# Optimization experiments

Hardware: AMD Instinct MI355X
Metric: run time of the kernel (lower is better)

Reference implementation:

```python
import jax, jax.numpy as jnp
import numpy as np

WS = 8        # window_size -> N = 64
P = 8         # patch_size
HEADS = 3
DIM = 96
B = 2048


def _relative_positions_log(ws):
    coords = jnp.stack(jnp.meshgrid(jnp.arange(ws), jnp.arange(ws), indexing='ij'))  # [2,ws,ws]
    cf = coords.reshape(2, -1)                                   # [2, N]
    rel = cf[:, :, None] - cf[:, None, :]                        # [2, N, N]
    rel = rel.transpose(1, 2, 0).astype(jnp.float32)             # [N, N, 2]
    return jnp.sign(rel) * jnp.log1p(jnp.abs(rel))


def setup_inputs() -> dict:
    key = jax.random.key(0)
    k0, k1, k2 = jax.random.split(key, 3)
    N = WS * WS
    qkv = jax.random.normal(k0, (B, N, 3 * DIM), dtype=jnp.float32)
    w1 = jax.random.normal(k1, (2, 256), dtype=jnp.float32) * 0.02
    b1 = jnp.zeros((256,), dtype=jnp.float32)
    w2 = jax.random.normal(k2, (256, HEADS), dtype=jnp.float32) * 0.02
    b2 = jnp.zeros((HEADS,), dtype=jnp.float32)
    return {"qkv": qkv, "w1": w1, "b1": b1, "w2": w2, "b2": b2}


def reference(qkv, w1, b1, w2, b2):
    B_, N, C3 = qkv.shape
    dim = C3 // 3
    h = HEADS
    d = dim // h
    scale = d ** (-0.5)

    qkv = qkv.reshape(B_, N, 3, h, d).transpose(2, 0, 3, 1, 4)   # [3,B,h,N,d]
    q, k, v = qkv[0] * scale, qkv[1], qkv[2]

    c = N // (P * P)
    def to_patch(x):  # [B,h,N,d] -> [B,h,c,d,P,P]
        return x.reshape(B_, h, c, P, P, d).transpose(0, 1, 2, 5, 3, 4)

    q_fft = jnp.fft.rfft2(to_patch(q))
    k_fft = jnp.fft.rfft2(to_patch(k))
    out = jnp.fft.irfft2(q_fft * k_fft, s=(P, P))                # [B,h,c,d,P,P]
    out = out.transpose(0, 1, 2, 4, 5, 3).reshape(B_, h, N, d)   # back to [B,h,N,d]

    rp = _relative_positions_log(WS)                             # [N,N,2]
    bias = jax.nn.relu(rp @ w1 + b1) @ w2 + b2                   # [N,N,h]
    bias = bias.transpose(2, 0, 1)                               # [h,N,N]

    attn = jnp.einsum('bhnd,bhmd->bhnm', out, v) + bias[None]
    attn = jax.nn.softmax(attn, axis=-1)
    x = jnp.einsum('bhnm,bhmd->bhnd', attn, v)
    return x.transpose(0, 2, 1, 3).reshape(B_, N, dim)
```

## Files before the change

kernel.cpp:

```cpp
#include <hip/hip_runtime.h>

#define B_TOT 2048
#define NHEAD 3

typedef __attribute__((ext_vector_type(8))) short short8v;
typedef __attribute__((ext_vector_type(4))) float f32x4;
typedef __attribute__((ext_vector_type(2))) __fp16 f16x2;

typedef __attribute__((address_space(1))) const void* gas_ptr;
typedef __attribute__((address_space(3))) void* las_ptr;

#define LOG2E 1.4426950408889634f

static __device__ __forceinline__ unsigned short f2bf(float x) {
    unsigned u = __builtin_bit_cast(unsigned, x);
    u += 0x7FFFu + ((u >> 16) & 1u);
    return (unsigned short)(u >> 16);
}
static __device__ __forceinline__ float bf2f(unsigned short s) {
    unsigned u = ((unsigned)s) << 16;
    return __builtin_bit_cast(float, u);
}
static __device__ __forceinline__ float exp2_fast(float x) {
    float r; asm("v_exp_f32 %0, %1" : "=v"(r) : "v"(x)); return r;
}

__global__ __launch_bounds__(256) void bias_kernel(const float* __restrict__ w1,
                                                   const float* __restrict__ b1,
                                                   const float* __restrict__ w2,
                                                   const float* __restrict__ b2,
                                                   float* __restrict__ bias2) {
    int gtid = blockIdx.x * 256 + threadIdx.x;
    int t = gtid >> 2, sub = gtid & 3;
    int h = t >> 12;
    int lane = (t >> 6) & 63;
    int pair = t & 63;
    int g = lane >> 4, c = lane & 15;
    int mt = pair >> 4, nt = (pair >> 2) & 3, r = pair & 3;
    int n = 16 * mt + 4 * g + r;
    int m = 16 * nt + c;

    float d0 = (float)((n >> 3) - (m >> 3));
    float d1 = (float)((n & 7) - (m & 7));
    float r0 = (d0 > 0.f ? 1.f : (d0 < 0.f ? -1.f : 0.f)) * log1pf(fabsf(d0));
    float r1 = (d1 > 0.f ? 1.f : (d1 < 0.f ? -1.f : 0.f)) * log1pf(fabsf(d1));
    float a = 0.f;
    for (int i = 0; i < 64; i++) {
        int j = 4 * i + sub;
        float hd = fmaf(r0, w1[j], fmaf(r1, w1[256 + j], b1[j]));
        hd = fmaxf(hd, 0.f);
        a = fmaf(hd, w2[j * 3 + h], a);
    }
    a += __shfl_xor(a, 1, 64);
    a += __shfl_xor(a, 2, 64);
    if (sub == 0)
        bias2[((h * 16 + mt * 4 + nt) * 64 + lane) * 4 + r] = (a + b2[h]) * LOG2E;
}

__global__ __launch_bounds__(256, 2) void attn_kernel(const float* __restrict__ qkv,
                                                      const float* __restrict__ bias2,
                                                      float* __restrict__ out) {
    __shared__ float smem[4][64 * 36];

    const int t = threadIdx.x;
    const int w = t >> 6;
    const int lane = t & 63;
    const int h = blockIdx.x % 3;
    const int b = (blockIdx.x / 3) * 4 + w;

    float* Qs = smem[w];
    const float* base = qkv + (size_t)b * (64 * 288) + h * 32;
    const float QS = 0.17677669529663687f * LOG2E;
    const int dd = lane & 31, H2 = lane >> 5;
    const int g = lane >> 4, c = lane & 15;
    const int nr = lane >> 3, d0q = (lane & 7) * 4;

    #pragma unroll
    for (int s = 0; s < 8; s++) {
        const float* gsrc = base + (8 * s + nr) * 288 + 96 + d0q;
        __builtin_amdgcn_global_load_lds((gas_ptr)gsrc, (las_ptr)(Qs + s * 256),
                                         16, 0, 0);
    }

    float4 qreg[8];
    #pragma unroll
    for (int s = 0; s < 8; s++)
        qreg[s] = *(const float4*)(base + (8 * s + nr) * 288 + d0q);

    asm volatile("s_waitcnt vmcnt(0)" ::: "memory");

    f16x2 krp[64];
    #pragma unroll
    for (int t8 = 0; t8 < 8; t8++) {
        const int rb = ((t8 + 4 * H2) & 7) * 8;
        float k8[8];
        #pragma unroll
        for (int tx = 0; tx < 8; tx++)
            k8[tx] = Qs[(rb + tx) * 32 + dd];
        #pragma unroll
        for (int i = 0; i < 8; i++)
            krp[t8 * 8 + i] = __builtin_amdgcn_cvt_pkrtz(k8[i], k8[(i - 1) & 7]);
    }
    __builtin_amdgcn_sched_barrier(0);

    #pragma unroll
    for (int s = 0; s < 8; s++) {
        float4 q4 = qreg[s];
        q4.x *= QS; q4.y *= QS; q4.z *= QS; q4.w *= QS;
        *(float4*)(Qs + (8 * s + nr) * 36 + d0q) = q4;
    }
    asm volatile("s_waitcnt lgkmcnt(0)" ::: "memory");

    float acc[4][8];
    #pragma unroll
    for (int yi = 0; yi < 4; yi++)
        #pragma unroll
        for (int x = 0; x < 8; x++) acc[yi][x] = 0.f;

    #pragma unroll
    for (int u = 0; u < 8; u++) {
        f16x2 q2[4];
        #pragma unroll
        for (int j = 0; j < 4; j++) {
            float qa = Qs[(u * 8 + 2 * j) * 36 + dd];
            float qb = Qs[(u * 8 + 2 * j + 1) * 36 + dd];
            q2[j] = __builtin_amdgcn_cvt_pkrtz(qa, qb);
        }
        #pragma unroll
        for (int yi = 0; yi < 4; yi++) {
            const int s = (yi - u) & 7;
            #pragma unroll
            for (int x = 0; x < 8; x++) {
                #pragma unroll
                for (int j = 0; j < 4; j++)
                    acc[yi][x] = __builtin_amdgcn_fdot2(
                        q2[j], krp[s * 8 + ((x - 2 * j) & 7)], acc[yi][x], false);
            }
        }
    }

    #pragma unroll
    for (int yi = 0; yi < 4; yi++) {
        const int n = (4 * H2 + yi) * 8;
        #pragma unroll
        for (int x = 0; x < 8; x++)
            Qs[(n + x) * 36 + dd] = acc[yi][x];
    }
    asm volatile("s_waitcnt lgkmcnt(0)" ::: "memory");

    short8v Oh[4], Ol[4];
    #pragma unroll
    for (int mt = 0; mt < 4; mt++) {
        const float* rp = Qs + (16 * mt + c) * 36 + 8 * g;
        float4 x0 = *(const float4*)rp;
        float4 x1 = *(const float4*)(rp + 4);
        float xs[8] = {x0.x, x0.y, x0.z, x0.w, x1.x, x1.y, x1.z, x1.w};
        #pragma unroll
        for (int j = 0; j < 8; j++) {
            unsigned short hb = f2bf(xs[j]);
            Oh[mt][j] = (short)hb;
            Ol[mt][j] = (short)f2bf(xs[j] - bf2f(hb));
        }
    }

    short8v Vh[4], Vl[4];
    #pragma unroll
    for (int nt = 0; nt < 4; nt++) {
        const float* vp = base + (16 * nt + c) * 288 + 192 + 8 * g;
        float4 x0 = *(const float4*)vp;
        float4 x1 = *(const float4*)(vp + 4);
        float xs[8] = {x0.x, x0.y, x0.z, x0.w, x1.x, x1.y, x1.z, x1.w};
        #pragma unroll
        for (int j = 0; j < 8; j++) {
            unsigned short hb = f2bf(xs[j]);
            Vh[nt][j] = (short)hb;
            Vl[nt][j] = (short)f2bf(xs[j] - bf2f(hb));
        }
    }

    const float* bb = bias2 + (size_t)h * 16 * 256 + lane * 4;
    f32x4 S[4][4];
    __builtin_amdgcn_s_setprio(1);
    #pragma unroll
    for (int mt = 0; mt < 4; mt++)
        #pragma unroll
        for (int nt = 0; nt < 4; nt++) {
            f32x4 a = __builtin_bit_cast(f32x4, *(const float4*)(bb + (mt * 4 + nt) * 256));
            a = __builtin_amdgcn_mfma_f32_16x16x32_bf16(Oh[mt], Vh[nt], a, 0, 0, 0);
            a = __builtin_amdgcn_mfma_f32_16x16x32_bf16(Oh[mt], Vl[nt], a, 0, 0, 0);
            a = __builtin_amdgcn_mfma_f32_16x16x32_bf16(Ol[mt], Vh[nt], a, 0, 0, 0);
            S[mt][nt] = a;
        }
    __builtin_amdgcn_s_setprio(0);

    float vb[2][2][8];
    #pragma unroll
    for (int kt = 0; kt < 2; kt++)
        #pragma unroll
        for (int dt = 0; dt < 2; dt++)
            #pragma unroll
            for (int j = 0; j < 8; j++)
                vb[kt][dt][j] = base[(32 * kt + 8 * g + j) * 288 + 192 + 16 * dt + c];

    #pragma unroll
    for (int mt = 0; mt < 4; mt++) {
        #pragma unroll
        for (int r = 0; r < 4; r++) {
            float m0 = fmaxf(fmaxf(S[mt][0][r], S[mt][1][r]), fmaxf(S[mt][2][r], S[mt][3][r]));
            m0 = fmaxf(m0, __shfl_xor(m0, 1, 64));
            m0 = fmaxf(m0, __shfl_xor(m0, 2, 64));
            m0 = fmaxf(m0, __shfl_xor(m0, 4, 64));
            m0 = fmaxf(m0, __shfl_xor(m0, 8, 64));
            #pragma unroll
            for (int nt = 0; nt < 4; nt++)
                S[mt][nt][r] = exp2_fast(S[mt][nt][r] - m0);
        }
    }

    unsigned short* Ps = (unsigned short*)Qs;
    #pragma unroll
    for (int mt = 0; mt < 4; mt++)
        #pragma unroll
        for (int nt = 0; nt < 4; nt++)
            #pragma unroll
            for (int r = 0; r < 4; r++)
                Ps[(16 * mt + 4 * g + r) * 72 + 16 * nt + c] = f2bf(S[mt][nt][r]);
    asm volatile("s_waitcnt lgkmcnt(0)" ::: "memory");

    short8v Pf[4][2];
    #pragma unroll
    for (int mt = 0; mt < 4; mt++)
        #pragma unroll
        for (int kt = 0; kt < 2; kt++)
            Pf[mt][kt] = *(const short8v*)(Ps + (16 * mt + c) * 72 + 32 * kt + 8 * g);

    short8v Vp[2][2];
    #pragma unroll
    for (int kt = 0; kt < 2; kt++)
        #pragma unroll
        for (int dt = 0; dt < 2; dt++)
            #pragma unroll
            for (int j = 0; j < 8; j++)
                Vp[kt][dt][j] = (short)f2bf(vb[kt][dt][j]);

    short8v ones;
    #pragma unroll
    for (int j = 0; j < 8; j++) ones[j] = (short)0x3F80;
    f32x4 inv4[4];
    __builtin_amdgcn_s_setprio(1);
    #pragma unroll
    for (int mt = 0; mt < 4; mt++) {
        f32x4 sa = {0.f, 0.f, 0.f, 0.f};
        sa = __builtin_amdgcn_mfma_f32_16x16x32_bf16(Pf[mt][0], ones, sa, 0, 0, 0);
        sa = __builtin_amdgcn_mfma_f32_16x16x32_bf16(Pf[mt][1], ones, sa, 0, 0, 0);
        #pragma unroll
        for (int r = 0; r < 4; r++) inv4[mt][r] = 1.f / sa[r];
    }

    f32x4 X[4][2];
    #pragma unroll
    for (int mt = 0; mt < 4; mt++)
        #pragma unroll
        for (int dt = 0; dt < 2; dt++) {
            f32x4 a = {0.f, 0.f, 0.f, 0.f};
            a = __builtin_amdgcn_mfma_f32_16x16x32_bf16(Pf[mt][0], Vp[0][dt], a, 0, 0, 0);
            a = __builtin_amdgcn_mfma_f32_16x16x32_bf16(Pf[mt][1], Vp[1][dt], a, 0, 0, 0);
            X[mt][dt] = a;
        }
    __builtin_amdgcn_s_setprio(0);

    float* op = out + (size_t)b * (64 * 96) + h * 32;
    #pragma unroll
    for (int mt = 0; mt < 4; mt++)
        #pragma unroll
        for (int dt = 0; dt < 2; dt++)
            #pragma unroll
            for (int r = 0; r < 4; r++)
                op[(16 * mt + 4 * g + r) * 96 + 16 * dt + c] = X[mt][dt][r] * inv4[mt][r];
}

extern "C" void kernel_launch(void* const* d_in, const int* in_sizes, int n_in,
                              void* d_out, int out_size, void* d_ws, size_t ws_size,
                              hipStream_t stream) {
    const float* qkv = (const float*)d_in[0];
    const float* w1  = (const float*)d_in[1];
    const float* b1  = (const float*)d_in[2];
    const float* w2  = (const float*)d_in[3];
    const float* b2  = (const float*)d_in[4];
    float* out = (float*)d_out;
    float* bias2 = (float*)d_ws;

    bias_kernel<<<192, 256, 0, stream>>>(w1, b1, w2, b2, bias2);
    attn_kernel<<<(B_TOT / 4) * NHEAD, 256, 0, stream>>>(qkv, bias2, out);
}
```

Before: 60.58 us.

## Stage V tile in LDS via async global_load_lds with XOR swizzle

V rows are now copied into a per-wave XOR-swizzled LDS buffer with global_load_lds, alongside K. Both the row-major and transposed V fragment reads then come from LDS instead of two separate global gathers, one of them strided. This cuts global memory traffic and uncoalesced scalar loads, at the cost of more LDS per block (occupancy risk at launch bounds of 2) and extra LDS reads.

```diff
diff --git a/kernel.cpp b/kernel.cpp
--- a/kernel.cpp
+++ b/kernel.cpp
@@ -60,7 +60,7 @@
 __global__ __launch_bounds__(256, 2) void attn_kernel(const float* __restrict__ qkv,
                                                       const float* __restrict__ bias2,
                                                       float* __restrict__ out) {
-    __shared__ float smem[4][64 * 36];
+    __shared__ float smem[4][2304 + 2048];
 
     const int t = threadIdx.x;
     const int w = t >> 6;
@@ -69,6 +69,7 @@
     const int b = (blockIdx.x / 3) * 4 + w;
 
     float* Qs = smem[w];
+    float* Vs = Qs + 2304;
     const float* base = qkv + (size_t)b * (64 * 288) + h * 32;
     const float QS = 0.17677669529663687f * LOG2E;
     const int dd = lane & 31, H2 = lane >> 5;
@@ -77,8 +78,11 @@
 
     #pragma unroll
     for (int s = 0; s < 8; s++) {
-        const float* gsrc = base + (8 * s + nr) * 288 + 96 + d0q;
-        __builtin_amdgcn_global_load_lds((gas_ptr)gsrc, (las_ptr)(Qs + s * 256),
+        const float* gk = base + (8 * s + nr) * 288 + 96 + d0q;
+        __builtin_amdgcn_global_load_lds((gas_ptr)gk, (las_ptr)(Qs + s * 256),
+                                         16, 0, 0);
+        const float* gv = base + (8 * s + nr) * 288 + 192 + (d0q ^ (4 * nr));
+        __builtin_amdgcn_global_load_lds((gas_ptr)gv, (las_ptr)(Vs + s * 256),
                                          16, 0, 0);
     }
 
@@ -164,17 +168,20 @@
     }
 
     short8v Vh[4], Vl[4];
-    #pragma unroll
-    for (int nt = 0; nt < 4; nt++) {
-        const float* vp = base + (16 * nt + c) * 288 + 192 + 8 * g;
-        float4 x0 = *(const float4*)vp;
-        float4 x1 = *(const float4*)(vp + 4);
-        float xs[8] = {x0.x, x0.y, x0.z, x0.w, x1.x, x1.y, x1.z, x1.w};
-        #pragma unroll
-        for (int j = 0; j < 8; j++) {
-            unsigned short hb = f2bf(xs[j]);
-            Vh[nt][j] = (short)hb;
-            Vl[nt][j] = (short)f2bf(xs[j] - bf2f(hb));
+    {
+        const int xorv = 4 * (c & 7);
+        #pragma unroll
+        for (int nt = 0; nt < 4; nt++) {
+            const float* rp = Vs + (16 * nt + c) * 32;
+            float4 x0 = *(const float4*)(rp + ((8 * g) ^ xorv));
+            float4 x1 = *(const float4*)(rp + ((8 * g + 4) ^ xorv));
+            float xs[8] = {x0.x, x0.y, x0.z, x0.w, x1.x, x1.y, x1.z, x1.w};
+            #pragma unroll
+            for (int j = 0; j < 8; j++) {
+                unsigned short hb = f2bf(xs[j]);
+                Vh[nt][j] = (short)hb;
+                Vl[nt][j] = (short)f2bf(xs[j] - bf2f(hb));
+            }
         }
     }
 
@@ -193,15 +200,6 @@
         }
     __builtin_amdgcn_s_setprio(0);
 
-    float vb[2][2][8];
-    #pragma unroll
-    for (int kt = 0; kt < 2; kt++)
-        #pragma unroll
-        for (int dt = 0; dt < 2; dt++)
-            #pragma unroll
-            for (int j = 0; j < 8; j++)
-                vb[kt][dt][j] = base[(32 * kt + 8 * g + j) * 288 + 192 + 16 * dt + c];
-
     #pragma unroll
     for (int mt = 0; mt < 4; mt++) {
         #pragma unroll
@@ -241,7 +239,8 @@
         for (int dt = 0; dt < 2; dt++)
             #pragma unroll
             for (int j = 0; j < 8; j++)
-                Vp[kt][dt][j] = (short)f2bf(vb[kt][dt][j]);
+                Vp[kt][dt][j] = (short)f2bf(
+                    Vs[(32 * kt + 8 * g + j) * 32 + ((16 * dt + c) ^ (4 * j))]);
 
     short8v ones;
     #pragma unroll
```

Result: slower. 66.99 us (+10.6%).
